# Optimization experiments

Measured on AMD Instinct MI355X. Metric: run time of the kernel, lower is better.

## Reference

```python
import jax, jax.numpy as jnp
import numpy as np

N = 100000
E = 3200000
DIM_IN, DIM_H, DIM_OUT = 256, 128, 64


def setup_inputs() -> dict:
    key = jax.random.key(0)
    k1, k2, k3, k4 = jax.random.split(key, 4)
    x = jax.random.normal(k1, (N, DIM_IN), dtype=jnp.float32)
    edge_index = jax.random.randint(k2, (2, E), 0, N, dtype=jnp.int32)
    # Glorot-ish init for the two GCNConv linear layers (weight + bias, PyG defaults)
    W1 = jax.random.normal(k3, (DIM_IN, DIM_H), dtype=jnp.float32) * (1.0 / np.sqrt(DIM_IN))
    b1 = jnp.zeros((DIM_H,), dtype=jnp.float32)
    W2 = jax.random.normal(k4, (DIM_H, DIM_OUT), dtype=jnp.float32) * (1.0 / np.sqrt(DIM_H))
    b2 = jnp.zeros((DIM_OUT,), dtype=jnp.float32)
    return {"x": x, "W1": W1, "b1": b1, "W2": W2, "b2": b2, "edge_index": edge_index}


def _gcn_norm(edge_index, num_nodes):
    """Add self-loops and compute symmetric D^{-1/2} A_hat D^{-1/2} edge weights."""
    loops = jnp.arange(num_nodes, dtype=edge_index.dtype)
    src = jnp.concatenate([edge_index[0], loops])
    dst = jnp.concatenate([edge_index[1], loops])
    deg = jax.ops.segment_sum(jnp.ones_like(dst, dtype=jnp.float32), dst,
                              num_segments=num_nodes)
    dinv = jnp.where(deg > 0, jax.lax.rsqrt(deg), 0.0)
    norm = dinv[src] * dinv[dst]  # [E + N]
    return src, dst, norm


def _gcn_conv(h, W, b, src, dst, norm, num_nodes):
    h = h @ W                                   # [N, F_out] linear transform first (PyG order)
    msg = norm[:, None] * h[src]                # gather + scale messages
    agg = jax.ops.segment_sum(msg, dst, num_segments=num_nodes)  # scatter-add
    return agg + b


def reference(x, W1, b1, W2, b2, edge_index):
    n = x.shape[0]
    src, dst, norm = _gcn_norm(edge_index, n)
    h = _gcn_conv(x, W1, b1, src, dst, norm, n)
    h = jax.nn.relu(h)
    h = _gcn_conv(h, W2, b2, src, dst, norm, n)
    return jax.nn.log_softmax(h, axis=1)
```

## Files before the change

kernel.cpp:

```cpp
#include <hip/hip_runtime.h>
#include <hip/hip_bf16.h>

#define WAVE 64
typedef unsigned int uint32;
typedef __attribute__((ext_vector_type(8))) short bf16x8;
typedef __attribute__((ext_vector_type(4))) float f32x4;
typedef __attribute__((ext_vector_type(2))) float f32x2;

__device__ inline uint32 f2bf(float f) {
    union { float f; uint32 u; } a; a.f = f;
    uint32 u = a.u;
    u += 0x7fffu + ((u >> 16) & 1u);
    return u >> 16;
}
__device__ inline uint32 packbf(float lo, float hi) { return f2bf(lo) | (f2bf(hi) << 16); }
__device__ inline short f2bfs(float f) { return (short)f2bf(f); }
__device__ inline f32x2 shflx(f32x2 v, int o) {
    v.x = __shfl_xor(v.x, o, WAVE);
    v.y = __shfl_xor(v.y, o, WAVE);
    return v;
}
template <bool HI>
__device__ inline f32x2 up8(uint32 u) {
    return __builtin_amdgcn_cvt_pk_f32_fp8((int)u, HI);
}
__device__ inline unsigned short pack8(float lo, float hi) {
    return (unsigned short)__builtin_amdgcn_cvt_pk_fp8_f32(lo, hi, 0, false);
}

__global__ void convert_w_kernel(const float* __restrict__ W1, const float* __restrict__ W2,
                                 uint32* __restrict__ w1f, uint32* __restrict__ w2f,
                                 int* __restrict__ gcnt) {
    int tid = blockIdx.x * blockDim.x + threadIdx.x;
    if (tid < 256) gcnt[tid] = 0;
    if (tid < 16384) {
        int w = tid & 3, l = (tid >> 2) & 63, c = (tid >> 8) & 7, kc = tid >> 11;
        int q = l & 15, g = l >> 4;
        int k0 = kc * 32 + g * 8 + 2 * w;
        int n = c * 16 + q;
        w1f[tid] = packbf(W1[k0 * 128 + n], W1[(k0 + 1) * 128 + n]);
    } else if (tid < 16384 + 4096) {
        int t = tid - 16384;
        int w = t & 3, l = (t >> 2) & 63, c = (t >> 8) & 3, kc = t >> 10;
        int q = l & 15, g = l >> 4;
        int k0 = kc * 32 + g * 8 + 2 * w;
        int n = c * 16 + q;
        w2f[t] = packbf(W2[k0 * 64 + n], W2[(k0 + 1) * 64 + n]);
    }
}

#define BIN_TB 1024
#define BIN_EPB 4096
__global__ __launch_bounds__(BIN_TB) void binsort_kernel(const int* __restrict__ src,
                                                         const int* __restrict__ dst,
                                                         int* __restrict__ gcnt,
                                                         uint32* __restrict__ pairs,
                                                         int E, int CAP) {
    __shared__ int hist[256];
    __shared__ int scan[256];
    __shared__ int lstart[256];
    __shared__ int gbase[256];
    __shared__ int lcur[256];
    __shared__ uint32 sp[BIN_EPB];
    __shared__ unsigned char sb[BIN_EPB];
    int tid = threadIdx.x;
    int base = blockIdx.x * BIN_EPB;
    if (tid < 256) hist[tid] = 0;
    __syncthreads();
    int s[4], b[4];
    uint32 pk[4];
    bool v[4];
#pragma unroll
    for (int j = 0; j < 4; ++j) {
        int e = base + tid + j * BIN_TB;
        v[j] = e < E;
        if (v[j]) {
            s[j] = src[e];
            int d = dst[e];
            b[j] = d >> 9;
            pk[j] = (uint32)s[j] | ((uint32)(d & 511) << 17);
            atomicAdd(&hist[b[j]], 1);
        }
    }
    __syncthreads();
    if (tid < 256) scan[tid] = hist[tid];
    __syncthreads();
#pragma unroll
    for (int o = 1; o < 256; o <<= 1) {
        int t = 0;
        if (tid < 256 && tid >= o) t = scan[tid - o];
        __syncthreads();
        if (tid < 256) scan[tid] += t;
        __syncthreads();
    }
    if (tid < 256) {
        int st = scan[tid] - hist[tid];
        lstart[tid] = st;
        lcur[tid] = st;
        gbase[tid] = (hist[tid] > 0) ? (tid * CAP + atomicAdd(&gcnt[tid], hist[tid])) : 0;
    }
    __syncthreads();
#pragma unroll
    for (int j = 0; j < 4; ++j) {
        if (v[j]) {
            int p = atomicAdd(&lcur[b[j]], 1);
            sp[p] = pk[j];
            sb[p] = (unsigned char)b[j];
        }
    }
    __syncthreads();
    int total = scan[255];
    for (int i = tid; i < total; i += BIN_TB) {
        int bb = sb[i];
        pairs[gbase[bb] + (i - lstart[bb])] = sp[i];
    }
}

__global__ __launch_bounds__(1024) void bucket_csr_kernel(const uint32* __restrict__ pairs,
                                                          const int* __restrict__ gcnt,
                                                          int* __restrict__ sorted,
                                                          int* __restrict__ rowstart,
                                                          int* __restrict__ rowend,
                                                          float* __restrict__ dinv,
                                                          int N, int CAP) {
    __shared__ int cnt[512];
    __shared__ int incl[512];
    __shared__ int cursor[512];
    extern __shared__ uint32 ssorted[];
    int b = blockIdx.x;
    int tid = threadIdx.x;
    int ne = gcnt[b];
    if (ne > CAP) ne = CAP;
    const uint32* P = pairs + (size_t)b * CAP;
    if (tid < 512) cnt[tid] = 0;
    __syncthreads();
    for (int i = tid; i < ne; i += 1024) atomicAdd(&cnt[P[i] >> 17], 1);
    __syncthreads();
    int v = 0;
    if (tid < 512) { v = cnt[tid]; incl[tid] = v; }
    __syncthreads();
#pragma unroll
    for (int o = 1; o < 512; o <<= 1) {
        int t = 0;
        if (tid < 512 && tid >= o) t = incl[tid - o];
        __syncthreads();
        if (tid < 512) incl[tid] += t;
        __syncthreads();
    }
    int gbase = b * CAP;
    if (tid < 512) {
        int node = b * 512 + tid;
        if (node < N) {
            rowstart[node] = gbase + incl[tid] - v;
            rowend[node] = gbase + incl[tid];
            dinv[node] = rsqrtf(1.0f + (float)v);
        }
        cursor[tid] = incl[tid] - v;
    }
    __syncthreads();
    for (int i = tid; i < ne; i += 1024) {
        uint32 p = P[i];
        int ln = p >> 17;
        int r = atomicAdd(&cursor[ln], 1);
        ssorted[r] = p & 0x1FFFFu;
    }
    __syncthreads();
    for (int i = tid; i < ne; i += 1024) sorted[gbase + i] = (int)ssorted[i];
}

__global__ __launch_bounds__(256) void gemm1_mfma(const float* __restrict__ x,
                                                  const uint32* __restrict__ w1f,
                                                  const float* __restrict__ dinv,
                                                  unsigned short* __restrict__ h1f,
                                                  int N) {
    const bf16x8* Bp = (const bf16x8*)w1f;
    int l = threadIdx.x & 63, w = threadIdx.x >> 6;
    int q = l & 15, g = l >> 4;
    int R = blockIdx.x * 128 + w * 32;
    f32x4 acc[2][8];
#pragma unroll
    for (int rt = 0; rt < 2; ++rt)
#pragma unroll
        for (int c = 0; c < 8; ++c) acc[rt][c] = (f32x4){0.f, 0.f, 0.f, 0.f};

#pragma unroll
    for (int kc = 0; kc < 8; ++kc) {
        bf16x8 b[8];
#pragma unroll
        for (int c = 0; c < 8; ++c) b[c] = Bp[(kc * 8 + c) * 64 + l];
#pragma unroll
        for (int rt = 0; rt < 2; ++rt) {
            int row = R + rt * 16 + q;
            row = row < N ? row : N - 1;
            const float* xr = x + (size_t)row * 256 + kc * 32 + g * 8;
            float4 xa = *(const float4*)xr;
            float4 xb = *(const float4*)(xr + 4);
            bf16x8 a;
            a[0] = f2bfs(xa.x); a[1] = f2bfs(xa.y); a[2] = f2bfs(xa.z); a[3] = f2bfs(xa.w);
            a[4] = f2bfs(xb.x); a[5] = f2bfs(xb.y); a[6] = f2bfs(xb.z); a[7] = f2bfs(xb.w);
#pragma unroll
            for (int c = 0; c < 8; ++c)
                acc[rt][c] = __builtin_amdgcn_mfma_f32_16x16x32_bf16(a, b[c], acc[rt][c], 0, 0, 0);
        }
    }
#pragma unroll
    for (int rt = 0; rt < 2; ++rt)
#pragma unroll
        for (int r = 0; r < 4; ++r) {
            int grow = R + rt * 16 + 4 * g + r;
            if (grow < N) {
                float wd = dinv[grow];
                unsigned short* orow = h1f + (size_t)grow * 64;
#pragma unroll
                for (int c = 0; c < 4; ++c)
                    orow[c * 16 + q] = pack8(acc[rt][c][r] * wd, acc[rt][c + 4][r] * wd);
            }
        }
}

__global__ __launch_bounds__(256) void agg1_kernel(const uint32* __restrict__ h1,
                                                   const float* __restrict__ dinv,
                                                   const int* __restrict__ srt,
                                                   const int* __restrict__ rowstart,
                                                   const int* __restrict__ rowend,
                                                   const float* __restrict__ bias,
                                                   uint32* __restrict__ out,
                                                   int n) {
    int wid = (int)(((long)blockIdx.x * blockDim.x + threadIdx.x) >> 6);
    int lane = threadIdx.x & 63;
    if (wid >= n) return;
    int q = lane & 31;
    int half = lane >> 5;
    int start = rowstart[wid];
    int end = rowend[wid];
    f32x2 aL = {0.f, 0.f}, aH = {0.f, 0.f};
    if (half == 0) {
        uint32 u = h1[(size_t)wid * 32 + q];
        aL = up8<false>(u); aH = up8<true>(u);
    }
    int e = start + half;
    for (; e + 6 < end; e += 8) {
        int s0 = srt[e], s1 = srt[e + 2], s2 = srt[e + 4], s3 = srt[e + 6];
        uint32 u0 = h1[(size_t)s0 * 32 + q];
        uint32 u1 = h1[(size_t)s1 * 32 + q];
        uint32 u2 = h1[(size_t)s2 * 32 + q];
        uint32 u3 = h1[(size_t)s3 * 32 + q];
        aL += up8<false>(u0); aH += up8<true>(u0);
        aL += up8<false>(u1); aH += up8<true>(u1);
        aL += up8<false>(u2); aH += up8<true>(u2);
        aL += up8<false>(u3); aH += up8<true>(u3);
    }
    for (; e < end; e += 2) {
        uint32 u = h1[(size_t)srt[e] * 32 + q];
        aL += up8<false>(u); aH += up8<true>(u);
    }
    aL += shflx(aL, 32);
    aH += shflx(aH, 32);
    if (half == 0) {
        float wd = dinv[wid];
        float2 b0 = ((const float2*)bias)[q];
        float2 b1 = ((const float2*)bias)[q + 32];
        float v0 = fmaxf(fmaf(wd, aL.x, b0.x), 0.f);
        float v1 = fmaxf(fmaf(wd, aH.x, b0.y), 0.f);
        float v2 = fmaxf(fmaf(wd, aL.y, b1.x), 0.f);
        float v3 = fmaxf(fmaf(wd, aH.y, b1.y), 0.f);
        uint32* orow = out + (size_t)wid * 64;
        orow[q] = packbf(v0, v1);
        orow[32 + q] = packbf(v2, v3);
    }
}

__global__ __launch_bounds__(256) void gemm2_mfma(const uint32* __restrict__ hin,
                                                  const uint32* __restrict__ w2f,
                                                  const float* __restrict__ dinv,
                                                  unsigned short* __restrict__ h2f,
                                                  int N) {
    const bf16x8* Bp = (const bf16x8*)w2f;
    const short* hs = (const short*)hin;
    int l = threadIdx.x & 63, w = threadIdx.x >> 6;
    int q = l & 15, g = l >> 4;
    int R = blockIdx.x * 128 + w * 32;
    f32x4 acc[2][4];
#pragma unroll
    for (int rt = 0; rt < 2; ++rt)
#pragma unroll
        for (int c = 0; c < 4; ++c) acc[rt][c] = (f32x4){0.f, 0.f, 0.f, 0.f};

#pragma unroll
    for (int kc = 0; kc < 4; ++kc) {
        bf16x8 b[4];
#pragma unroll
        for (int c = 0; c < 4; ++c) b[c] = Bp[(kc * 4 + c) * 64 + l];
#pragma unroll
        for (int rt = 0; rt < 2; ++rt) {
            int row = R + rt * 16 + q;
            row = row < N ? row : N - 1;
            bf16x8 a = *(const bf16x8*)(hs + (size_t)row * 128 + kc * 32 + g * 8);
#pragma unroll
            for (int c = 0; c < 4; ++c)
                acc[rt][c] = __builtin_amdgcn_mfma_f32_16x16x32_bf16(a, b[c], acc[rt][c], 0, 0, 0);
        }
    }
#pragma unroll
    for (int rt = 0; rt < 2; ++rt)
#pragma unroll
        for (int r = 0; r < 4; ++r) {
            int grow = R + rt * 16 + 4 * g + r;
            if (grow < N) {
                float wd = dinv[grow];
                unsigned short* orow = h2f + (size_t)grow * 32;
#pragma unroll
                for (int c = 0; c < 2; ++c)
                    orow[c * 16 + q] = pack8(acc[rt][c][r] * wd, acc[rt][c + 2][r] * wd);
            }
        }
}

__global__ __launch_bounds__(256) void agg2_ls_kernel(const uint32* __restrict__ h2,
                                                      const float* __restrict__ dinv,
                                                      const int* __restrict__ srt,
                                                      const int* __restrict__ rowstart,
                                                      const int* __restrict__ rowend,
                                                      const float* __restrict__ bias,
                                                      float* __restrict__ out, int n) {
    int wid = (int)(((long)blockIdx.x * blockDim.x + threadIdx.x) >> 6);
    int lane = threadIdx.x & 63;
    if (wid >= n) return;
    int q = lane & 15;
    int g = lane >> 4;
    int start = rowstart[wid];
    int end = rowend[wid];
    f32x2 aL = {0.f, 0.f}, aH = {0.f, 0.f};
    if (g == 0) {
        uint32 u = h2[(size_t)wid * 16 + q];
        aL = up8<false>(u); aH = up8<true>(u);
    }
    int e = start + g;
    for (; e + 12 < end; e += 16) {
        int s0 = srt[e], s1 = srt[e + 4], s2 = srt[e + 8], s3 = srt[e + 12];
        uint32 u0 = h2[(size_t)s0 * 16 + q];
        uint32 u1 = h2[(size_t)s1 * 16 + q];
        uint32 u2 = h2[(size_t)s2 * 16 + q];
        uint32 u3 = h2[(size_t)s3 * 16 + q];
        aL += up8<false>(u0); aH += up8<true>(u0);
        aL += up8<false>(u1); aH += up8<true>(u1);
        aL += up8<false>(u2); aH += up8<true>(u2);
        aL += up8<false>(u3); aH += up8<true>(u3);
    }
    for (; e < end; e += 4) {
        uint32 u = h2[(size_t)srt[e] * 16 + q];
        aL += up8<false>(u); aH += up8<true>(u);
    }
    aL += shflx(aL, 16); aH += shflx(aH, 16);
    aL += shflx(aL, 32); aH += shflx(aH, 32);
    float wd = dinv[wid];
    float2 b0 = ((const float2*)bias)[q];
    float2 b1 = ((const float2*)bias)[q + 16];
    float v0 = fmaf(wd, aL.x, b0.x);
    float v1 = fmaf(wd, aH.x, b0.y);
    float v2 = fmaf(wd, aL.y, b1.x);
    float v3 = fmaf(wd, aH.y, b1.y);
    float m = fmaxf(fmaxf(v0, v1), fmaxf(v2, v3));
#pragma unroll
    for (int o = 1; o <= 8; o <<= 1) m = fmaxf(m, __shfl_xor(m, o, WAVE));
    float s = __expf(v0 - m) + __expf(v1 - m) + __expf(v2 - m) + __expf(v3 - m);
#pragma unroll
    for (int o = 1; o <= 8; o <<= 1) s += __shfl_xor(s, o, WAVE);
    float lg = __logf(s) + m;
    if (g == 0) {
        *(float2*)&out[(size_t)wid * 64 + 2 * q] = make_float2(v0 - lg, v1 - lg);
        *(float2*)&out[(size_t)wid * 64 + 32 + 2 * q] = make_float2(v2 - lg, v3 - lg);
    }
}

extern "C" void kernel_launch(void* const* d_in, const int* in_sizes, int n_in,
                              void* d_out, int out_size, void* d_ws, size_t ws_size,
                              hipStream_t stream) {
    const float* x  = (const float*)d_in[0];
    const float* W1 = (const float*)d_in[1];
    const float* b1 = (const float*)d_in[2];
    const float* W2 = (const float*)d_in[3];
    const float* b2 = (const float*)d_in[4];
    const int* edge = (const int*)d_in[5];

    const int N = in_sizes[0] / 256;
    const int E = in_sizes[5] / 2;
    const int* src = edge;
    const int* dst = edge + E;

    const int NBUCK = (N + 511) >> 9;
    int mean = E / NBUCK;
    int CAP = mean + (int)(8.5 * __builtin_sqrt((double)mean)) + 32;
    CAP = (CAP + 63) & ~63;
    if (CAP > 36864) CAP = 36864;

    int*    gcnt     = (int*)d_ws;
    uint32* w1f      = (uint32*)(gcnt + 256);
    uint32* w2f      = w1f + 16384;
    float*  dinv     = (float*)(w2f + 4096);
    int*    rowstart = (int*)(dinv + N);
    int*    rowend   = rowstart + N;
    int*    sorted   = rowend + N;
    uint32* h1f      = (uint32*)(sorted + (size_t)NBUCK * CAP);
    uint32* h2f      = h1f + (size_t)N * 32;
    uint32* agg1bf   = h2f + (size_t)N * 16;
    uint32* pairs    = agg1bf;
    float*  outp     = (float*)d_out;

    const int TB = 256;

    convert_w_kernel<<<80, TB, 0, stream>>>(W1, W2, w1f, w2f, gcnt);

    binsort_kernel<<<(E + BIN_EPB - 1) / BIN_EPB, BIN_TB, 0, stream>>>(src, dst, gcnt, pairs, E, CAP);
    bucket_csr_kernel<<<NBUCK, 1024, (size_t)CAP * 4, stream>>>(pairs, gcnt, sorted, rowstart, rowend, dinv, N, CAP);

    gemm1_mfma<<<(N + 127) / 128, TB, 0, stream>>>(x, w1f, dinv, (unsigned short*)h1f, N);

    agg1_kernel<<<(N * 64 + TB - 1) / TB, TB, 0, stream>>>(h1f, dinv, sorted, rowstart, rowend, b1, agg1bf, N);

    gemm2_mfma<<<(N + 127) / 128, TB, 0, stream>>>(agg1bf, w2f, dinv, (unsigned short*)h2f, N);

    agg2_ls_kernel<<<(N * 64 + TB - 1) / TB, TB, 0, stream>>>(h2f, dinv, sorted, rowstart, rowend, b2, outp, N);
}
```

Baseline: 219.8 us.

## Halve bucket size, stage bf16 x tiles in LDS, unroll gathers deeper

Bucket width drops from 512 to 256 nodes, which doubles the number of buckets and halves CAP, so each bucket CSR block needs less shared memory and more blocks run at once. gemm1 now converts x to bf16 cooperatively into an LDS tile with coalesced loads, replacing the strided per-lane global reads. Both aggregation kernels unroll their edge gather loops from 4 to 8 loads for more memory-level parallelism. The risks are extra barriers in gemm1, a longer 512-entry scan in binsort, and overflow if a bucket exceeds the new CAP.

```diff
diff --git a/kernel.cpp b/kernel.cpp
--- a/kernel.cpp
+++ b/kernel.cpp
@@ -14,7 +14,6 @@
     return u >> 16;
 }
 __device__ inline uint32 packbf(float lo, float hi) { return f2bf(lo) | (f2bf(hi) << 16); }
-__device__ inline short f2bfs(float f) { return (short)f2bf(f); }
 __device__ inline f32x2 shflx(f32x2 v, int o) {
     v.x = __shfl_xor(v.x, o, WAVE);
     v.y = __shfl_xor(v.y, o, WAVE);
@@ -32,7 +31,7 @@
                                  uint32* __restrict__ w1f, uint32* __restrict__ w2f,
                                  int* __restrict__ gcnt) {
     int tid = blockIdx.x * blockDim.x + threadIdx.x;
-    if (tid < 256) gcnt[tid] = 0;
+    if (tid < 512) gcnt[tid] = 0;
     if (tid < 16384) {
         int w = tid & 3, l = (tid >> 2) & 63, c = (tid >> 8) & 7, kc = tid >> 11;
         int q = l & 15, g = l >> 4;
@@ -56,18 +55,18 @@
                                                          int* __restrict__ gcnt,
                                                          uint32* __restrict__ pairs,
                                                          int E, int CAP) {
-    __shared__ int hist[256];
-    __shared__ int scan[256];
-    __shared__ int lstart[256];
-    __shared__ int gbase[256];
-    __shared__ int lcur[256];
+    __shared__ int hist[512];
+    __shared__ int scan[512];
+    __shared__ int lstart[512];
+    __shared__ int gbase[512];
+    __shared__ int lcur[512];
     __shared__ uint32 sp[BIN_EPB];
-    __shared__ unsigned char sb[BIN_EPB];
+    __shared__ unsigned short sb[BIN_EPB];
     int tid = threadIdx.x;
     int base = blockIdx.x * BIN_EPB;
-    if (tid < 256) hist[tid] = 0;
-    __syncthreads();
-    int s[4], b[4];
+    if (tid < 512) hist[tid] = 0;
+    __syncthreads();
+    int b[4];
     uint32 pk[4];
     bool v[4];
 #pragma unroll
@@ -75,25 +74,25 @@
         int e = base + tid + j * BIN_TB;
         v[j] = e < E;
         if (v[j]) {
-            s[j] = src[e];
+            int s = src[e];
             int d = dst[e];
-            b[j] = d >> 9;
-            pk[j] = (uint32)s[j] | ((uint32)(d & 511) << 17);
+            b[j] = d >> 8;
+            pk[j] = (uint32)s | ((uint32)(d & 255) << 17);
             atomicAdd(&hist[b[j]], 1);
         }
     }
     __syncthreads();
-    if (tid < 256) scan[tid] = hist[tid];
-    __syncthreads();
-#pragma unroll
-    for (int o = 1; o < 256; o <<= 1) {
+    if (tid < 512) scan[tid] = hist[tid];
+    __syncthreads();
+#pragma unroll
+    for (int o = 1; o < 512; o <<= 1) {
         int t = 0;
-        if (tid < 256 && tid >= o) t = scan[tid - o];
-        __syncthreads();
-        if (tid < 256) scan[tid] += t;
-        __syncthreads();
-    }
-    if (tid < 256) {
+        if (tid < 512 && tid >= o) t = scan[tid - o];
+        __syncthreads();
+        if (tid < 512) scan[tid] += t;
+        __syncthreads();
+    }
+    if (tid < 512) {
         int st = scan[tid] - hist[tid];
         lstart[tid] = st;
         lcur[tid] = st;
@@ -105,11 +104,11 @@
         if (v[j]) {
             int p = atomicAdd(&lcur[b[j]], 1);
             sp[p] = pk[j];
-            sb[p] = (unsigned char)b[j];
-        }
-    }
-    __syncthreads();
-    int total = scan[255];
+            sb[p] = (unsigned short)b[j];
+        }
+    }
+    __syncthreads();
+    int total = scan[511];
     for (int i = tid; i < total; i += BIN_TB) {
         int bb = sb[i];
         pairs[gbase[bb] + (i - lstart[bb])] = sp[i];
@@ -123,33 +122,33 @@
                                                           int* __restrict__ rowend,
                                                           float* __restrict__ dinv,
                                                           int N, int CAP) {
-    __shared__ int cnt[512];
-    __shared__ int incl[512];
-    __shared__ int cursor[512];
+    __shared__ int cnt[256];
+    __shared__ int incl[256];
+    __shared__ int cursor[256];
     extern __shared__ uint32 ssorted[];
     int b = blockIdx.x;
     int tid = threadIdx.x;
     int ne = gcnt[b];
     if (ne > CAP) ne = CAP;
     const uint32* P = pairs + (size_t)b * CAP;
-    if (tid < 512) cnt[tid] = 0;
+    if (tid < 256) cnt[tid] = 0;
     __syncthreads();
     for (int i = tid; i < ne; i += 1024) atomicAdd(&cnt[P[i] >> 17], 1);
     __syncthreads();
     int v = 0;
-    if (tid < 512) { v = cnt[tid]; incl[tid] = v; }
-    __syncthreads();
-#pragma unroll
-    for (int o = 1; o < 512; o <<= 1) {
+    if (tid < 256) { v = cnt[tid]; incl[tid] = v; }
+    __syncthreads();
+#pragma unroll
+    for (int o = 1; o < 256; o <<= 1) {
         int t = 0;
-        if (tid < 512 && tid >= o) t = incl[tid - o];
-        __syncthreads();
-        if (tid < 512) incl[tid] += t;
+        if (tid < 256 && tid >= o) t = incl[tid - o];
+        __syncthreads();
+        if (tid < 256) incl[tid] += t;
         __syncthreads();
     }
     int gbase = b * CAP;
-    if (tid < 512) {
-        int node = b * 512 + tid;
+    if (tid < 256) {
+        int node = b * 256 + tid;
         if (node < N) {
             rowstart[node] = gbase + incl[tid] - v;
             rowend[node] = gbase + incl[tid];
@@ -173,31 +172,44 @@
                                                   const float* __restrict__ dinv,
                                                   unsigned short* __restrict__ h1f,
                                                   int N) {
+    __shared__ short xs[128 * 40];
     const bf16x8* Bp = (const bf16x8*)w1f;
-    int l = threadIdx.x & 63, w = threadIdx.x >> 6;
+    int tid = threadIdx.x;
+    int l = tid & 63, w = tid >> 6;
     int q = l & 15, g = l >> 4;
-    int R = blockIdx.x * 128 + w * 32;
+    int R = blockIdx.x * 128;
+    int rloc = w * 32;
     f32x4 acc[2][8];
 #pragma unroll
     for (int rt = 0; rt < 2; ++rt)
 #pragma unroll
         for (int c = 0; c < 8; ++c) acc[rt][c] = (f32x4){0.f, 0.f, 0.f, 0.f};
 
+    int srow = tid >> 1;
+    int scol = (tid & 1) * 16;
+    long grow_s = R + srow;
+    if (grow_s > N - 1) grow_s = N - 1;
+    const float* xbase = x + grow_s * 256 + scol;
+    uint2* sdst = (uint2*)&xs[srow * 40 + scol];
+
 #pragma unroll
     for (int kc = 0; kc < 8; ++kc) {
+        __syncthreads();
+        {
+            const float4* xp = (const float4*)(xbase + kc * 32);
+            float4 f0 = xp[0], f1 = xp[1], f2 = xp[2], f3 = xp[3];
+            sdst[0] = make_uint2(packbf(f0.x, f0.y), packbf(f0.z, f0.w));
+            sdst[1] = make_uint2(packbf(f1.x, f1.y), packbf(f1.z, f1.w));
+            sdst[2] = make_uint2(packbf(f2.x, f2.y), packbf(f2.z, f2.w));
+            sdst[3] = make_uint2(packbf(f3.x, f3.y), packbf(f3.z, f3.w));
+        }
+        __syncthreads();
         bf16x8 b[8];
 #pragma unroll
         for (int c = 0; c < 8; ++c) b[c] = Bp[(kc * 8 + c) * 64 + l];
 #pragma unroll
         for (int rt = 0; rt < 2; ++rt) {
-            int row = R + rt * 16 + q;
-            row = row < N ? row : N - 1;
-            const float* xr = x + (size_t)row * 256 + kc * 32 + g * 8;
-            float4 xa = *(const float4*)xr;
-            float4 xb = *(const float4*)(xr + 4);
-            bf16x8 a;
-            a[0] = f2bfs(xa.x); a[1] = f2bfs(xa.y); a[2] = f2bfs(xa.z); a[3] = f2bfs(xa.w);
-            a[4] = f2bfs(xb.x); a[5] = f2bfs(xb.y); a[6] = f2bfs(xb.z); a[7] = f2bfs(xb.w);
+            bf16x8 a = *(const bf16x8*)&xs[(rloc + rt * 16 + q) * 40 + g * 8];
 #pragma unroll
             for (int c = 0; c < 8; ++c)
                 acc[rt][c] = __builtin_amdgcn_mfma_f32_16x16x32_bf16(a, b[c], acc[rt][c], 0, 0, 0);
@@ -207,7 +219,7 @@
     for (int rt = 0; rt < 2; ++rt)
 #pragma unroll
         for (int r = 0; r < 4; ++r) {
-            int grow = R + rt * 16 + 4 * g + r;
+            int grow = R + rloc + rt * 16 + 4 * g + r;
             if (grow < N) {
                 float wd = dinv[grow];
                 unsigned short* orow = h1f + (size_t)grow * 64;
@@ -239,16 +251,25 @@
         aL = up8<false>(u); aH = up8<true>(u);
     }
     int e = start + half;
-    for (; e + 6 < end; e += 8) {
+    for (; e + 14 < end; e += 16) {
         int s0 = srt[e], s1 = srt[e + 2], s2 = srt[e + 4], s3 = srt[e + 6];
+        int s4 = srt[e + 8], s5 = srt[e + 10], s6 = srt[e + 12], s7 = srt[e + 14];
         uint32 u0 = h1[(size_t)s0 * 32 + q];
         uint32 u1 = h1[(size_t)s1 * 32 + q];
         uint32 u2 = h1[(size_t)s2 * 32 + q];
         uint32 u3 = h1[(size_t)s3 * 32 + q];
+        uint32 u4 = h1[(size_t)s4 * 32 + q];
+        uint32 u5 = h1[(size_t)s5 * 32 + q];
+        uint32 u6 = h1[(size_t)s6 * 32 + q];
+        uint32 u7 = h1[(size_t)s7 * 32 + q];
         aL += up8<false>(u0); aH += up8<true>(u0);
         aL += up8<false>(u1); aH += up8<true>(u1);
         aL += up8<false>(u2); aH += up8<true>(u2);
         aL += up8<false>(u3); aH += up8<true>(u3);
+        aL += up8<false>(u4); aH += up8<true>(u4);
+        aL += up8<false>(u5); aH += up8<true>(u5);
+        aL += up8<false>(u6); aH += up8<true>(u6);
+        aL += up8<false>(u7); aH += up8<true>(u7);
     }
     for (; e < end; e += 2) {
         uint32 u = h1[(size_t)srt[e] * 32 + q];
@@ -336,16 +357,25 @@
         aL = up8<false>(u); aH = up8<true>(u);
     }
     int e = start + g;
-    for (; e + 12 < end; e += 16) {
+    for (; e + 28 < end; e += 32) {
         int s0 = srt[e], s1 = srt[e + 4], s2 = srt[e + 8], s3 = srt[e + 12];
+        int s4 = srt[e + 16], s5 = srt[e + 20], s6 = srt[e + 24], s7 = srt[e + 28];
         uint32 u0 = h2[(size_t)s0 * 16 + q];
         uint32 u1 = h2[(size_t)s1 * 16 + q];
         uint32 u2 = h2[(size_t)s2 * 16 + q];
         uint32 u3 = h2[(size_t)s3 * 16 + q];
+        uint32 u4 = h2[(size_t)s4 * 16 + q];
+        uint32 u5 = h2[(size_t)s5 * 16 + q];
+        uint32 u6 = h2[(size_t)s6 * 16 + q];
+        uint32 u7 = h2[(size_t)s7 * 16 + q];
         aL += up8<false>(u0); aH += up8<true>(u0);
         aL += up8<false>(u1); aH += up8<true>(u1);
         aL += up8<false>(u2); aH += up8<true>(u2);
         aL += up8<false>(u3); aH += up8<true>(u3);
+        aL += up8<false>(u4); aH += up8<true>(u4);
+        aL += up8<false>(u5); aH += up8<true>(u5);
+        aL += up8<false>(u6); aH += up8<true>(u6);
+        aL += up8<false>(u7); aH += up8<true>(u7);
     }
     for (; e < end; e += 4) {
         uint32 u = h2[(size_t)srt[e] * 16 + q];
@@ -388,14 +418,14 @@
     const int* src = edge;
     const int* dst = edge + E;
 
-    const int NBUCK = (N + 511) >> 9;
+    const int NBUCK = (N + 255) >> 8;
     int mean = E / NBUCK;
     int CAP = mean + (int)(8.5 * __builtin_sqrt((double)mean)) + 32;
     CAP = (CAP + 63) & ~63;
-    if (CAP > 36864) CAP = 36864;
+    if (CAP > 14336) CAP = 14336;
 
     int*    gcnt     = (int*)d_ws;
-    uint32* w1f      = (uint32*)(gcnt + 256);
+    uint32* w1f      = (uint32*)(gcnt + 512);
     uint32* w2f      = w1f + 16384;
     float*  dinv     = (float*)(w2f + 4096);
     int*    rowstart = (int*)(dinv + N);
```

Result: slower. 230.4 us (+4.9%).
